# Kernel optimization log

Hardware: AMD Instinct MI355X
Metric: run time of the kernel (lower is better)

The kernel has to match this reference:

```python
import jax, jax.numpy as jnp
import numpy as np

COST_CLASS = 1.0


def _lsa(cost):
    """linear_sum_assignment clone (Jonker-Volgenant shortest augmenting path),
    matching scipy.optimize.linear_sum_assignment semantics for rectangular inputs."""
    cost = np.asarray(cost, dtype=np.float64)
    transposed = cost.shape[0] > cost.shape[1]
    if transposed:
        cost = cost.T
    nr, nc = cost.shape
    u = np.zeros(nr)
    v = np.zeros(nc)
    path = np.full(nc, -1, dtype=np.int64)
    col4row = np.full(nr, -1, dtype=np.int64)
    row4col = np.full(nc, -1, dtype=np.int64)
    for cur in range(nr):
        i = cur
        SR = np.zeros(nr, dtype=bool)
        SC = np.zeros(nc, dtype=bool)
        d = np.full(nc, np.inf)
        minVal = 0.0
        sink = -1
        while sink == -1:
            SR[i] = True
            rem = ~SC
            r = minVal + cost[i, rem] - u[i] - v[rem]
            dr = d[rem]
            pr = path[rem]
            better = r < dr
            dr[better] = r[better]
            pr[better] = i
            d[rem] = dr
            path[rem] = pr
            remIdx = np.flatnonzero(rem)
            j = remIdx[np.argmin(d[remIdx])]
            minVal = d[j]
            SC[j] = True
            if row4col[j] == -1:
                sink = j
            else:
                i = row4col[j]
        # dual updates (scipy _lsap_body)
        u[cur] += minVal
        mask = SR.copy()
        mask[cur] = False
        u[mask] += minVal - d[col4row[mask]]
        v[SC] -= minVal - d[SC]
        # augment along shortest path
        j = sink
        while True:
            i = path[j]
            row4col[j] = i
            col4row[i], j = j, col4row[i]
            if i == cur:
                break
    if transposed:
        order = np.argsort(col4row)
        return col4row[order], order
    return np.arange(nr), col4row


def setup_inputs() -> dict:
    key = jax.random.key(0)
    k1, k2, k3 = jax.random.split(key, 3)
    bs, Q, T, NC = 32, 256, 128, 2048
    pred_logits = jax.random.normal(k1, (bs, Q, NC), dtype=jnp.float32)
    tgt_labels = jax.random.randint(k2, (bs, T), 0, NC)
    agent_mask = jax.random.randint(k3, (bs, Q), 0, 2).astype(bool)
    return {"pred_logits": pred_logits, "tgt_labels": tgt_labels,
            "agent_mask": agent_mask, "use_background": 0}


def reference(pred_logits, tgt_labels, agent_mask, use_background):
    bs, Q, _ = pred_logits.shape
    T = tgt_labels.shape[1]
    probs = jax.nn.softmax(pred_logits, axis=-1)  # [bs, Q, NC]
    if not use_background:
        probs = jnp.where(agent_mask[:, :, None], probs, 0.0)
    out_prob = probs.reshape(bs * Q, -1)
    tgt_ids = tgt_labels.reshape(-1)                  # concat of all batch labels
    C = COST_CLASS * (-out_prob[:, tgt_ids])          # [bs*Q, bs*T]
    C = C.reshape(bs, Q, bs * T)
    # per-batch Hungarian (same as scipy loop in the original; inherently serial per instance)
    Cn = np.asarray(C)
    rows = np.empty((bs, T), dtype=np.int64)
    cols = np.empty((bs, T), dtype=np.int64)
    for i in range(bs):
        r, c = _lsa(Cn[i, :, i * T:(i + 1) * T])      # [Q, T] block for batch i
        rows[i] = r
        cols[i] = c
    return C, jnp.asarray(rows), jnp.asarray(cols)
```

## Files before the change

### kernel.cpp

```cpp
#include <hip/hip_runtime.h>
#include <hip/hip_bf16.h>
#include <math.h>

#define BS 32
#define QN 256
#define TN 128
#define NCLS 2048
#define NTGT (BS * TN)

__global__ void detect_mask_layout(const unsigned char* __restrict__ m, int* flag) {
    __shared__ int found;
    if (threadIdx.x == 0) found = 0;
    __syncthreads();
    int local = 0;
    for (int i = threadIdx.x; i < BS * QN; i += blockDim.x) {
        if ((i & 3) != 0 && m[i] != 0) local = 1;
    }
    if (local) atomicOr(&found, 1);
    __syncthreads();
    if (threadIdx.x == 0) *flag = found;
}

__global__ __launch_bounds__(256) void compute_C_kernel(
    const float* __restrict__ logits, const int* __restrict__ labels,
    const unsigned char* __restrict__ mask_b, const int* __restrict__ use_bg,
    const int* __restrict__ layout_flag, float* __restrict__ C) {
    __shared__ float prob_sh[NCLS];
    __shared__ int lab_sh[NTGT];
    __shared__ float red[4];

    const int tid = threadIdx.x;
    const int bq = blockIdx.x;
    const float* row = logits + (size_t)bq * NCLS;

    for (int k = tid; k < NTGT; k += 256) lab_sh[k] = labels[k];

    float x[8];
    float m = -INFINITY;
#pragma unroll
    for (int k = 0; k < 8; k++) {
        x[k] = row[tid + k * 256];
        m = fmaxf(m, x[k]);
    }
#pragma unroll
    for (int off = 32; off >= 1; off >>= 1) m = fmaxf(m, __shfl_xor(m, off));
    if ((tid & 63) == 0) red[tid >> 6] = m;
    __syncthreads();
    m = fmaxf(fmaxf(red[0], red[1]), fmaxf(red[2], red[3]));
    __syncthreads();

    float e[8];
    float s = 0.f;
#pragma unroll
    for (int k = 0; k < 8; k++) {
        e[k] = expf(x[k] - m);
        s += e[k];
    }
#pragma unroll
    for (int off = 32; off >= 1; off >>= 1) s += __shfl_xor(s, off);
    if ((tid & 63) == 0) red[tid >> 6] = s;
    __syncthreads();
    s = ((red[0] + red[1]) + red[2]) + red[3];

#pragma unroll
    for (int k = 0; k < 8; k++) prob_sh[tid + k * 256] = e[k] / s;

    const int ub = *use_bg;
    int am;
    if (*layout_flag)
        am = mask_b[bq];
    else
        am = ((const int*)mask_b)[bq];
    const bool zero_row = (ub == 0) && (am == 0);
    __syncthreads();

    float* Crow = C + (size_t)bq * NTGT;
#pragma unroll
    for (int k = 0; k < 16; k++) {
        const int jj = tid + k * 256;
        Crow[jj] = zero_row ? 0.0f : -prob_sh[lab_sh[jj]];
    }
}

__global__ __launch_bounds__(256) void transpose_kernel(const float* __restrict__ C,
                                                        float* __restrict__ CT) {
    __shared__ float tile[TN][65];
    const int b = blockIdx.x;
    const int q0 = blockIdx.y * 64;
    const int tid = threadIdx.x;

    const float* src = C + (size_t)(b * QN + q0) * NTGT + b * TN;
#pragma unroll
    for (int it = 0; it < 32; it++) {
        const int idx = tid + it * 256;
        const int ql = idx >> 7;
        const int i = idx & 127;
        tile[i][ql] = src[(size_t)ql * NTGT + i];
    }
    __syncthreads();
    float* dst = CT + (size_t)b * TN * QN + q0;
#pragma unroll
    for (int it = 0; it < 32; it++) {
        const int idx = tid + it * 256;
        const int i = idx >> 6;
        const int ql = idx & 63;
        dst[(size_t)i * QN + ql] = tile[i][ql];
    }
}

template <int CTRL>
__device__ __forceinline__ double dpp_mov_f64(double x) {
    union { double d; int i[2]; } a, r;
    a.d = x;
    r.i[0] = __builtin_amdgcn_update_dpp(0, a.i[0], CTRL, 0xF, 0xF, true);
    r.i[1] = __builtin_amdgcn_update_dpp(0, a.i[1], CTRL, 0xF, 0xF, true);
    return r.d;
}
__device__ __forceinline__ double read_lane_f64(double x, int srclane) {
    union { double d; int i[2]; } a, r;
    a.d = x;
    r.i[0] = __builtin_amdgcn_readlane(a.i[0], srclane);
    r.i[1] = __builtin_amdgcn_readlane(a.i[1], srclane);
    return r.d;
}

#define QUAD_XOR1 0xB1
#define QUAD_XOR2 0x4E
#define ROW_ROR4  0x124
#define ROW_ROR8  0x128

__global__ __launch_bounds__(64) void lsa_kernel(const float* __restrict__ C,
                                                 const float* __restrict__ CT,
                                                 float* __restrict__ rows_out,
                                                 float* __restrict__ cols_out) {
    const int b = blockIdx.x;
    const int lane = threadIdx.x;
    const int j0 = lane * 4;

    __shared__ float cost_sh[TN * QN];
    __shared__ double u_sh[TN];
    __shared__ int path_sh[QN];
    __shared__ int row4col_sh[QN];
    __shared__ int col4row_sh[TN];

    u_sh[lane] = 0.0;
    u_sh[lane + 64] = 0.0;
    col4row_sh[lane] = -1;
    col4row_sh[lane + 64] = -1;
#pragma unroll
    for (int t = 0; t < 4; t++) row4col_sh[lane + 64 * t] = -1;

    double v0 = 0.0, v1 = 0.0, v2 = 0.0, v3 = 0.0;
    double u0 = 0.0, u1 = 0.0;

    if (CT) {
        const float4* src = (const float4*)(CT + (size_t)b * TN * QN);
        float4* dst = (float4*)cost_sh;
#pragma unroll 8
        for (int it = 0; it < TN * QN / 4 / 64; it++) {
            const int idx = it * 64 + lane;
            dst[idx] = src[idx];
        }
    } else {
        const float* cbsrc = C + (size_t)b * QN * NTGT + b * TN;
        for (int it = 0; it < 512; it++) {
            const int j = it >> 1;
            const int i = lane + 64 * (it & 1);
            cost_sh[i * QN + j] = cbsrc[(size_t)j * NTGT + i];
        }
    }
    __syncthreads();

    for (int cur = 0; cur < TN; cur++) {
        double dv0 = INFINITY, dv1 = INFINITY, dv2 = INFINITY, dv3 = INFINITY;
        double dm0 = INFINITY, dm1 = INFINITY, dm2 = INFINITY, dm3 = INFINITY;
        double du0 = 0.0, du1 = 0.0;
        int sc = 0, sr = 0;
        int p0 = 0, p1 = 0, p2 = 0, p3 = 0;
        const int4 rcv = *(const int4*)&row4col_sh[j0];
        if (lane == (cur >> 1)) sr = 1 << (cur & 1);

        int i = cur;
        double m_d = 0.0;
        bool need_reduce = true;
        unsigned long long B0 = 0, B1 = 0, B2 = 0, B3 = 0;
        int sink;

        while (true) {
            const float4 cc = *(const float4*)(cost_sh + i * QN + j0);
            const double ui = u_sh[i];

            const double ca0 = ((m_d + (double)cc.x) - ui) - v0;
            const double ca1 = ((m_d + (double)cc.y) - ui) - v1;
            const double ca2 = ((m_d + (double)cc.z) - ui) - v2;
            const double ca3 = ((m_d + (double)cc.w) - ui) - v3;
            const bool i0 = !(sc & 1) && (ca0 < dv0);
            const bool i1 = !(sc & 2) && (ca1 < dv1);
            const bool i2 = !(sc & 4) && (ca2 < dv2);
            const bool i3 = !(sc & 8) && (ca3 < dv3);
            const unsigned long long anyI =
                __ballot(i0) | __ballot(i1) | __ballot(i2) | __ballot(i3);
            if (i0) { dv0 = ca0; dm0 = ca0; p0 = i; }
            if (i1) { dv1 = ca1; dm1 = ca1; p1 = i; }
            if (i2) { dv2 = ca2; dm2 = ca2; p2 = i; }
            if (i3) { dv3 = ca3; dm3 = ca3; p3 = i; }

            if (anyI != 0ull || need_reduce) {
                double lm = fmin(fmin(dm0, dm1), fmin(dm2, dm3));
                lm = fmin(lm, dpp_mov_f64<QUAD_XOR1>(lm));
                lm = fmin(lm, dpp_mov_f64<QUAD_XOR2>(lm));
                lm = fmin(lm, dpp_mov_f64<ROW_ROR4>(lm));
                lm = fmin(lm, dpp_mov_f64<ROW_ROR8>(lm));
                const double r0 = read_lane_f64(lm, 0);
                const double r1 = read_lane_f64(lm, 16);
                const double r2 = read_lane_f64(lm, 32);
                const double r3 = read_lane_f64(lm, 48);
                m_d = fmin(fmin(r0, r1), fmin(r2, r3));
                B0 = __ballot(dm0 == m_d);
                B1 = __ballot(dm1 == m_d);
                B2 = __ballot(dm2 == m_d);
                B3 = __ballot(dm3 == m_d);
            }

            int jmin = 0x7fffffff;
            if (B0) { const int c = ((__ffsll((long long)B0) - 1) << 2) + 0; jmin = c < jmin ? c : jmin; }
            if (B1) { const int c = ((__ffsll((long long)B1) - 1) << 2) + 1; jmin = c < jmin ? c : jmin; }
            if (B2) { const int c = ((__ffsll((long long)B2) - 1) << 2) + 2; jmin = c < jmin ? c : jmin; }
            if (B3) { const int c = ((__ffsll((long long)B3) - 1) << 2) + 3; jmin = c < jmin ? c : jmin; }
            const int owner = jmin >> 2;
            const int slot = jmin & 3;
            const unsigned long long bit = 1ull << owner;
            if (slot == 0) B0 &= ~bit;
            else if (slot == 1) B1 &= ~bit;
            else if (slot == 2) B2 &= ~bit;
            else B3 &= ~bit;

            if (lane == owner) {
                sc |= 1 << slot;
                if (slot == 0) dm0 = INFINITY;
                else if (slot == 1) dm1 = INFINITY;
                else if (slot == 2) dm2 = INFINITY;
                else dm3 = INFINITY;
            }

            const int sa = (slot & 1) ? rcv.y : rcv.x;
            const int sb = (slot & 1) ? rcv.w : rcv.z;
            const int rcsel = (slot & 2) ? sb : sa;
            const int krc = __builtin_amdgcn_readlane(rcsel, owner);
            if (krc < 0) { sink = jmin; break; }

            if (lane == (krc >> 1)) {
                if (krc & 1) { du1 = m_d; sr |= 2; }
                else { du0 = m_d; sr |= 1; }
            }
            i = krc;
            need_reduce = ((B0 | B1 | B2 | B3) == 0ull);
        }

        path_sh[lane] = p0;
        path_sh[lane + 64] = p1;
        path_sh[lane + 128] = p2;
        path_sh[lane + 192] = p3;
        if (sc & 1) v0 -= m_d - dv0;
        if (sc & 2) v1 -= m_d - dv1;
        if (sc & 4) v2 -= m_d - dv2;
        if (sc & 8) v3 -= m_d - dv3;
        if (sr & 1) u0 += (2 * lane == cur) ? m_d : (m_d - du0);
        if (sr & 2) u1 += (2 * lane + 1 == cur) ? m_d : (m_d - du1);
        u_sh[2 * lane] = u0;
        u_sh[2 * lane + 1] = u1;
        __syncthreads();

        if (lane == 0) {
            int j = sink;
            while (true) {
                const int pi = path_sh[(j & 3) * 64 + (j >> 2)];
                row4col_sh[j] = pi;
                const int nj = col4row_sh[pi];
                col4row_sh[pi] = j;
                j = nj;
                if (pi == cur) break;
            }
        }
        __syncthreads();
    }

#pragma unroll
    for (int t = 0; t < 2; t++) {
        const int ii = lane + 64 * t;
        const int myv = col4row_sh[ii];
        int rank = 0;
        for (int t2 = 0; t2 < TN; t2++) rank += (col4row_sh[t2] < myv) ? 1 : 0;
        rows_out[b * TN + rank] = (float)myv;
        cols_out[b * TN + rank] = (float)ii;
    }
}

extern "C" void kernel_launch(void* const* d_in, const int* in_sizes, int n_in,
                              void* d_out, int out_size, void* d_ws, size_t ws_size,
                              hipStream_t stream) {
    const float* logits = (const float*)d_in[0];
    const int* labels = (const int*)d_in[1];
    const unsigned char* mask_b = (const unsigned char*)d_in[2];
    const int* use_bg = (const int*)d_in[3];

    float* C = (float*)d_out;
    float* rows_out = C + (size_t)BS * QN * NTGT;
    float* cols_out = rows_out + BS * TN;

    int* flag = (int*)d_ws;
    const size_t ct_off = 4096;
    const size_t ct_bytes = (size_t)BS * TN * QN * sizeof(float);
    const bool useCT = ws_size >= ct_off + ct_bytes;
    float* CT = useCT ? (float*)((char*)d_ws + ct_off) : nullptr;

    detect_mask_layout<<<1, 256, 0, stream>>>(mask_b, flag);
    compute_C_kernel<<<BS * QN, 256, 0, stream>>>(logits, labels, mask_b, use_bg, flag, C);
    if (useCT) {
        dim3 tg(BS, QN / 64);
        transpose_kernel<<<tg, 256, 0, stream>>>(C, CT);
    }
    lsa_kernel<<<BS, 64, 0, stream>>>(C, CT, rows_out, cols_out);
}
```

Before: 1.152 ms.

## Keep LSA dual/assignment state in registers and speculatively prefetch next row

Moves u, row4col, col4row and path state from shared memory into per-lane registers, accessed via readlane, so the augmentation runs wave-wide without __syncthreads or a single-lane shared-memory loop. Adds a speculative path: when tied minima remain, the next row's cost and u are prefetched and the wave-wide min reduction is skipped if no newly relaxed column falls at or below the current minimum. This cuts LDS round-trips, barriers and reductions on the serial Hungarian critical path, at the cost of extra readlanes, an extra LDS load per step and more register pressure.

```diff
diff --git a/kernel.cpp b/kernel.cpp
--- a/kernel.cpp
+++ b/kernel.cpp
@@ -123,11 +123,34 @@
     r.i[1] = __builtin_amdgcn_readlane(a.i[1], srclane);
     return r.d;
 }
+__device__ __forceinline__ double read_u_reg(double u0, double u1, int i) {
+    union { double d; int i2[2]; } a0, a1, r;
+    a0.d = u0;
+    a1.d = u1;
+    const int ow = i >> 1;
+    const int lo0 = __builtin_amdgcn_readlane(a0.i2[0], ow);
+    const int hi0 = __builtin_amdgcn_readlane(a0.i2[1], ow);
+    const int lo1 = __builtin_amdgcn_readlane(a1.i2[0], ow);
+    const int hi1 = __builtin_amdgcn_readlane(a1.i2[1], ow);
+    r.i2[0] = (i & 1) ? lo1 : lo0;
+    r.i2[1] = (i & 1) ? hi1 : hi0;
+    return r.d;
+}
 
 #define QUAD_XOR1 0xB1
 #define QUAD_XOR2 0x4E
 #define ROW_ROR4  0x124
 #define ROW_ROR8  0x128
+
+__device__ __forceinline__ int first_tied(unsigned long long B0, unsigned long long B1,
+                                          unsigned long long B2, unsigned long long B3) {
+    int jmin = 0x7fffffff;
+    if (B0) { const int c = ((__ffsll((long long)B0) - 1) << 2) + 0; jmin = c < jmin ? c : jmin; }
+    if (B1) { const int c = ((__ffsll((long long)B1) - 1) << 2) + 1; jmin = c < jmin ? c : jmin; }
+    if (B2) { const int c = ((__ffsll((long long)B2) - 1) << 2) + 2; jmin = c < jmin ? c : jmin; }
+    if (B3) { const int c = ((__ffsll((long long)B3) - 1) << 2) + 3; jmin = c < jmin ? c : jmin; }
+    return jmin;
+}
 
 __global__ __launch_bounds__(64) void lsa_kernel(const float* __restrict__ C,
                                                  const float* __restrict__ CT,
@@ -138,20 +161,7 @@
     const int j0 = lane * 4;
 
     __shared__ float cost_sh[TN * QN];
-    __shared__ double u_sh[TN];
-    __shared__ int path_sh[QN];
-    __shared__ int row4col_sh[QN];
     __shared__ int col4row_sh[TN];
-
-    u_sh[lane] = 0.0;
-    u_sh[lane + 64] = 0.0;
-    col4row_sh[lane] = -1;
-    col4row_sh[lane + 64] = -1;
-#pragma unroll
-    for (int t = 0; t < 4; t++) row4col_sh[lane + 64 * t] = -1;
-
-    double v0 = 0.0, v1 = 0.0, v2 = 0.0, v3 = 0.0;
-    double u0 = 0.0, u1 = 0.0;
 
     if (CT) {
         const float4* src = (const float4*)(CT + (size_t)b * TN * QN);
@@ -171,24 +181,41 @@
     }
     __syncthreads();
 
+    double v0 = 0.0, v1 = 0.0, v2 = 0.0, v3 = 0.0;
+    double u0 = 0.0, u1 = 0.0;
+    int rc0 = -1, rc1 = -1, rc2 = -1, rc3 = -1;
+    int cr0 = -1, cr1 = -1;
+
     for (int cur = 0; cur < TN; cur++) {
         double dv0 = INFINITY, dv1 = INFINITY, dv2 = INFINITY, dv3 = INFINITY;
         double dm0 = INFINITY, dm1 = INFINITY, dm2 = INFINITY, dm3 = INFINITY;
-        double du0 = 0.0, du1 = 0.0;
+        double duA = 0.0, duB = 0.0;
         int sc = 0, sr = 0;
         int p0 = 0, p1 = 0, p2 = 0, p3 = 0;
-        const int4 rcv = *(const int4*)&row4col_sh[j0];
         if (lane == (cur >> 1)) sr = 1 << (cur & 1);
 
         int i = cur;
         double m_d = 0.0;
-        bool need_reduce = true;
         unsigned long long B0 = 0, B1 = 0, B2 = 0, B3 = 0;
-        int sink;
+        int sink = 0;
+
+        float4 cc = *(const float4*)(cost_sh + i * QN + j0);
+        double ui = read_u_reg(u0, u1, i);
 
         while (true) {
-            const float4 cc = *(const float4*)(cost_sh + i * QN + j0);
-            const double ui = u_sh[i];
+            const unsigned long long Ball = B0 | B1 | B2 | B3;
+            int jspec = 0, sowner = 0, sslot = 0, krcspec = -1;
+            int ispec = 0;
+            if (Ball) {
+                jspec = first_tied(B0, B1, B2, B3);
+                sowner = jspec >> 2;
+                sslot = jspec & 3;
+                const int rsel = (sslot == 0) ? rc0 : (sslot == 1) ? rc1 : (sslot == 2) ? rc2 : rc3;
+                krcspec = __builtin_amdgcn_readlane(rsel, sowner);
+                ispec = krcspec >= 0 ? krcspec : 0;
+            }
+            const float4 ccs = *(const float4*)(cost_sh + ispec * QN + j0);
+            const double uis = read_u_reg(u0, u1, ispec);
 
             const double ca0 = ((m_d + (double)cc.x) - ui) - v0;
             const double ca1 = ((m_d + (double)cc.y) - ui) - v1;
@@ -198,35 +225,54 @@
             const bool i1 = !(sc & 2) && (ca1 < dv1);
             const bool i2 = !(sc & 4) && (ca2 < dv2);
             const bool i3 = !(sc & 8) && (ca3 < dv3);
-            const unsigned long long anyI =
-                __ballot(i0) | __ballot(i1) | __ballot(i2) | __ballot(i3);
+            const unsigned long long chk =
+                __ballot(i0 && (ca0 <= m_d)) | __ballot(i1 && (ca1 <= m_d)) |
+                __ballot(i2 && (ca2 <= m_d)) | __ballot(i3 && (ca3 <= m_d));
             if (i0) { dv0 = ca0; dm0 = ca0; p0 = i; }
             if (i1) { dv1 = ca1; dm1 = ca1; p1 = i; }
             if (i2) { dv2 = ca2; dm2 = ca2; p2 = i; }
             if (i3) { dv3 = ca3; dm3 = ca3; p3 = i; }
 
-            if (anyI != 0ull || need_reduce) {
-                double lm = fmin(fmin(dm0, dm1), fmin(dm2, dm3));
-                lm = fmin(lm, dpp_mov_f64<QUAD_XOR1>(lm));
-                lm = fmin(lm, dpp_mov_f64<QUAD_XOR2>(lm));
-                lm = fmin(lm, dpp_mov_f64<ROW_ROR4>(lm));
-                lm = fmin(lm, dpp_mov_f64<ROW_ROR8>(lm));
-                const double r0 = read_lane_f64(lm, 0);
-                const double r1 = read_lane_f64(lm, 16);
-                const double r2 = read_lane_f64(lm, 32);
-                const double r3 = read_lane_f64(lm, 48);
-                m_d = fmin(fmin(r0, r1), fmin(r2, r3));
-                B0 = __ballot(dm0 == m_d);
-                B1 = __ballot(dm1 == m_d);
-                B2 = __ballot(dm2 == m_d);
-                B3 = __ballot(dm3 == m_d);
-            }
-
-            int jmin = 0x7fffffff;
-            if (B0) { const int c = ((__ffsll((long long)B0) - 1) << 2) + 0; jmin = c < jmin ? c : jmin; }
-            if (B1) { const int c = ((__ffsll((long long)B1) - 1) << 2) + 1; jmin = c < jmin ? c : jmin; }
-            if (B2) { const int c = ((__ffsll((long long)B2) - 1) << 2) + 2; jmin = c < jmin ? c : jmin; }
-            if (B3) { const int c = ((__ffsll((long long)B3) - 1) << 2) + 3; jmin = c < jmin ? c : jmin; }
+            if (chk == 0ull && Ball) {
+                const unsigned long long bit = 1ull << sowner;
+                if (sslot == 0) B0 &= ~bit;
+                else if (sslot == 1) B1 &= ~bit;
+                else if (sslot == 2) B2 &= ~bit;
+                else B3 &= ~bit;
+                if (krcspec < 0) { sink = jspec; break; }
+                if (lane == sowner) {
+                    sc |= 1 << sslot;
+                    if (sslot == 0) dm0 = INFINITY;
+                    else if (sslot == 1) dm1 = INFINITY;
+                    else if (sslot == 2) dm2 = INFINITY;
+                    else dm3 = INFINITY;
+                }
+                if (lane == (krcspec >> 1)) {
+                    if (krcspec & 1) { duB = m_d; sr |= 2; }
+                    else { duA = m_d; sr |= 1; }
+                }
+                i = krcspec;
+                cc = ccs;
+                ui = uis;
+                continue;
+            }
+
+            double lm = fmin(fmin(dm0, dm1), fmin(dm2, dm3));
+            lm = fmin(lm, dpp_mov_f64<QUAD_XOR1>(lm));
+            lm = fmin(lm, dpp_mov_f64<QUAD_XOR2>(lm));
+            lm = fmin(lm, dpp_mov_f64<ROW_ROR4>(lm));
+            lm = fmin(lm, dpp_mov_f64<ROW_ROR8>(lm));
+            const double r0 = read_lane_f64(lm, 0);
+            const double r1 = read_lane_f64(lm, 16);
+            const double r2 = read_lane_f64(lm, 32);
+            const double r3 = read_lane_f64(lm, 48);
+            m_d = fmin(fmin(r0, r1), fmin(r2, r3));
+            B0 = __ballot(dm0 == m_d);
+            B1 = __ballot(dm1 == m_d);
+            B2 = __ballot(dm2 == m_d);
+            B3 = __ballot(dm3 == m_d);
+
+            const int jmin = first_tied(B0, B1, B2, B3);
             const int owner = jmin >> 2;
             const int slot = jmin & 3;
             const unsigned long long bit = 1ull << owner;
@@ -234,7 +280,9 @@
             else if (slot == 1) B1 &= ~bit;
             else if (slot == 2) B2 &= ~bit;
             else B3 &= ~bit;
-
+            const int rsel2 = (slot == 0) ? rc0 : (slot == 1) ? rc1 : (slot == 2) ? rc2 : rc3;
+            const int krc = __builtin_amdgcn_readlane(rsel2, owner);
+            if (krc < 0) { sink = jmin; break; }
             if (lane == owner) {
                 sc |= 1 << slot;
                 if (slot == 0) dm0 = INFINITY;
@@ -242,53 +290,54 @@
                 else if (slot == 2) dm2 = INFINITY;
                 else dm3 = INFINITY;
             }
-
-            const int sa = (slot & 1) ? rcv.y : rcv.x;
-            const int sb = (slot & 1) ? rcv.w : rcv.z;
-            const int rcsel = (slot & 2) ? sb : sa;
-            const int krc = __builtin_amdgcn_readlane(rcsel, owner);
-            if (krc < 0) { sink = jmin; break; }
-
             if (lane == (krc >> 1)) {
-                if (krc & 1) { du1 = m_d; sr |= 2; }
-                else { du0 = m_d; sr |= 1; }
+                if (krc & 1) { duB = m_d; sr |= 2; }
+                else { duA = m_d; sr |= 1; }
             }
             i = krc;
-            need_reduce = ((B0 | B1 | B2 | B3) == 0ull);
+            cc = *(const float4*)(cost_sh + i * QN + j0);
+            ui = read_u_reg(u0, u1, i);
         }
 
-        path_sh[lane] = p0;
-        path_sh[lane + 64] = p1;
-        path_sh[lane + 128] = p2;
-        path_sh[lane + 192] = p3;
         if (sc & 1) v0 -= m_d - dv0;
         if (sc & 2) v1 -= m_d - dv1;
         if (sc & 4) v2 -= m_d - dv2;
         if (sc & 8) v3 -= m_d - dv3;
-        if (sr & 1) u0 += (2 * lane == cur) ? m_d : (m_d - du0);
-        if (sr & 2) u1 += (2 * lane + 1 == cur) ? m_d : (m_d - du1);
-        u_sh[2 * lane] = u0;
-        u_sh[2 * lane + 1] = u1;
-        __syncthreads();
-
-        if (lane == 0) {
-            int j = sink;
-            while (true) {
-                const int pi = path_sh[(j & 3) * 64 + (j >> 2)];
-                row4col_sh[j] = pi;
-                const int nj = col4row_sh[pi];
-                col4row_sh[pi] = j;
-                j = nj;
-                if (pi == cur) break;
-            }
+        if (sr & 1) u0 += (2 * lane == cur) ? m_d : (m_d - duA);
+        if (sr & 2) u1 += (2 * lane + 1 == cur) ? m_d : (m_d - duB);
+
+        int j = sink;
+        while (true) {
+            const int aslot = j & 3;
+            const int aowner = j >> 2;
+            const int psel = (aslot == 0) ? p0 : (aslot == 1) ? p1 : (aslot == 2) ? p2 : p3;
+            const int pi = __builtin_amdgcn_readlane(psel, aowner);
+            if (lane == aowner) {
+                if (aslot == 0) rc0 = pi;
+                else if (aslot == 1) rc1 = pi;
+                else if (aslot == 2) rc2 = pi;
+                else rc3 = pi;
+            }
+            const int cowner = pi >> 1;
+            const int cslot = pi & 1;
+            const int csel = cslot ? cr1 : cr0;
+            const int nj = __builtin_amdgcn_readlane(csel, cowner);
+            if (lane == cowner) {
+                if (cslot) cr1 = j;
+                else cr0 = j;
+            }
+            j = nj;
+            if (pi == cur) break;
         }
-        __syncthreads();
-    }
-
+    }
+
+    col4row_sh[2 * lane] = cr0;
+    col4row_sh[2 * lane + 1] = cr1;
+    __syncthreads();
 #pragma unroll
     for (int t = 0; t < 2; t++) {
-        const int ii = lane + 64 * t;
-        const int myv = col4row_sh[ii];
+        const int ii = 2 * lane + t;
+        const int myv = t ? cr1 : cr0;
         int rank = 0;
         for (int t2 = 0; t2 < TN; t2++) rank += (col4row_sh[t2] < myv) ? 1 : 0;
         rows_out[b * TN + rank] = (float)myv;
```

After: 1.394 ms. 1.21x slower.
